# Kernel optimization log

Measured on AMD Instinct MI355X. Metric: run time of the kernel, lower is better.

Reference implementation:

```python
import jax, jax.numpy as jnp
import numpy as np

NODE_NUM = 256  # nodes per env block; N = NODE_NUM * n_thr
N, MAX_DEG, N_FEAT, N_HID, N_CLASS = 8192, 16, 128, 256, 64


def _xavier_uniform(key, fan_in, fan_out, gain=1.414):
    limit = gain * np.sqrt(6.0 / (fan_in + fan_out))
    return jax.random.uniform(key, (fan_in, fan_out), jnp.float32, -limit, limit)


def setup_inputs() -> dict:
    key = jax.random.key(0)
    k1, k2, k3, k4 = jax.random.split(key, 4)
    x = jax.random.normal(k1, (N, N_FEAT), jnp.float32)
    edge_index = jax.random.randint(k2, (N, MAX_DEG), 0, NODE_NUM)  # local neighbor ids, -1 = pad
    W1 = _xavier_uniform(k3, N_FEAT, N_HID)
    W2 = _xavier_uniform(k4, N_HID, N_CLASS)
    return {"x": x, "edge_index": edge_index, "W1": W1, "W2": W2}


def build_adj(edge_index, node_num):
    # Vectorized version of the nested-Python-loop to_adj scatter.
    n, d = edge_index.shape
    rows = jnp.broadcast_to(jnp.arange(n)[:, None], (n, d))  # [N, D]
    cols = edge_index + node_num * (rows // node_num)        # global neighbor index
    valid = (edge_index != -1).astype(jnp.float32)
    # .max with 0 for invalid entries is a no-op regardless of the (wrapped) index,
    # exactly reproducing "set adj[i, j_ind] = 1 only when j != -1".
    adj = jnp.zeros((n, n), jnp.float32).at[rows.ravel(), cols.ravel()].max(valid.ravel())
    return adj


def reference(x, edge_index, W1, W2):
    adj = build_adj(edge_index, NODE_NUM)            # [N, N]
    h = jax.nn.relu(adj @ (x @ W1))                  # gc1 + relu (dropout is identity at eval)
    out = adj @ (h @ W2)                             # gc2
    return jax.nn.log_softmax(out, axis=1)
```

## Files before the change

kernel.cpp:

```cpp
#include <hip/hip_runtime.h>
#include <math.h>

#define NNODES   8192
#define NODE_NUM 256
#define MAX_DEG  16
#define N_FEAT   128
#define N_HID    256
#define N_CLASS  64

#define AG_STRIDE 136
#define HB_STRIDE 264

typedef __attribute__((ext_vector_type(8))) short bf16x8;
typedef __attribute__((ext_vector_type(4))) short s16x4;
typedef __attribute__((ext_vector_type(4))) float f32x4;

static __device__ __forceinline__ short f2b(float f) {
    unsigned u = __float_as_uint(f);
    unsigned r = (u + 0x7fffu + ((u >> 16) & 1u)) >> 16;
    return (short)r;
}
static __device__ __forceinline__ float b2f(short s) {
    return __uint_as_float(((unsigned)(unsigned short)s) << 16);
}

__global__ __launch_bounds__(256) void k_prep(const int* __restrict__ edge,
                                              const float* __restrict__ W1,
                                              const float* __restrict__ W2,
                                              unsigned int* __restrict__ maskw,
                                              short* __restrict__ W1T,
                                              short* __restrict__ W2T) {
    const int g = blockIdx.x * 256 + threadIdx.x;
    if (g < 8192) {
        const int* e = edge + (size_t)g * MAX_DEG;
        int ids[MAX_DEG];
#pragma unroll
        for (int k = 0; k < MAX_DEG; ++k) ids[k] = e[k];
        unsigned m = 0;
#pragma unroll
        for (int k = 0; k < MAX_DEG; ++k) {
            bool skip = (ids[k] == -1);
#pragma unroll
            for (int q = 0; q < k; ++q) skip = skip || (ids[q] == ids[k]);
            if (!skip) m |= 1u << k;
        }
        maskw[g] = m;
    } else if (g < 40960) {
        const int o = g - 8192;
        const int j = o & 7, l = (o >> 3) & 63, k4 = (o >> 9) & 3, nt = (o >> 11) & 15;
        W1T[o] = f2b(W1[(k4 * 32 + (l >> 4) * 8 + j) * N_HID + nt * 16 + (l & 15)]);
    } else if (g < 57344) {
        const int o = g - 40960;
        const int j = o & 7, l = (o >> 3) & 63, k8 = (o >> 9) & 7, nt = (o >> 12) & 3;
        W2T[o] = f2b(W2[(k8 * 32 + (l >> 4) * 8 + j) * N_CLASS + nt * 16 + (l & 15)]);
    }
}

__global__ __launch_bounds__(512) void k_main(const float* __restrict__ x,
                                              const int* __restrict__ edge,
                                              const unsigned int* __restrict__ maskw,
                                              const short* __restrict__ W1T,
                                              const short* __restrict__ W2T,
                                              short* __restrict__ t2b) {
    __shared__ short agg[32 * AG_STRIDE];
    __shared__ short hb[32 * HB_STRIDE];

    const int bid  = blockIdx.x;
    const int work = (bid & 7) * 32 + (bid >> 3);
    const int row0 = work * 32;
    const int t    = threadIdx.x;
    const int w    = t >> 6, l = t & 63;
    const int l16  = l & 15, l4 = l >> 4;

    bf16x8 w1f[4][4];
    {
        const int ntb = (w & 3) * 4;
#pragma unroll
        for (int n = 0; n < 4; ++n)
#pragma unroll
            for (int k4 = 0; k4 < 4; ++k4)
                w1f[n][k4] = *(const bf16x8*)(W1T + ((size_t)((ntb + n) * 4 + k4) * 64 + l) * 8);
    }
    bf16x8 w2f[8];
    {
        const int nt = w & 3;
#pragma unroll
        for (int k8 = 0; k8 < 8; ++k8)
            w2f[k8] = *(const bf16x8*)(W2T + ((size_t)(nt * 8 + k8) * 64 + l) * 8);
    }

    {
        const int r = t >> 4, c = t & 15;
        const int node = row0 + r;
        const int base = node & ~(NODE_NUM - 1);
        const int* e = edge + (size_t)node * MAX_DEG;
        const unsigned m = maskw[node];
        float a[8] = {0, 0, 0, 0, 0, 0, 0, 0};
#pragma unroll
        for (int k = 0; k < MAX_DEG; ++k) {
            const int id = e[k] & (NODE_NUM - 1);
            const float sel = ((m >> k) & 1u) ? 1.0f : 0.0f;
            const float* rowp = x + (size_t)(base + id) * N_FEAT + c * 8;
            float4 v0 = *(const float4*)(rowp);
            float4 v1 = *(const float4*)(rowp + 4);
            a[0] = fmaf(sel, v0.x, a[0]); a[1] = fmaf(sel, v0.y, a[1]);
            a[2] = fmaf(sel, v0.z, a[2]); a[3] = fmaf(sel, v0.w, a[3]);
            a[4] = fmaf(sel, v1.x, a[4]); a[5] = fmaf(sel, v1.y, a[5]);
            a[6] = fmaf(sel, v1.z, a[6]); a[7] = fmaf(sel, v1.w, a[7]);
        }
        bf16x8 p;
#pragma unroll
        for (int j = 0; j < 8; ++j) p[j] = f2b(a[j]);
        *(bf16x8*)(&agg[r * AG_STRIDE + c * 8]) = p;
    }
    __syncthreads();

    const int mt = w >> 2, ntc = w & 3;
    {
        bf16x8 af[4];
#pragma unroll
        for (int k4 = 0; k4 < 4; ++k4)
            af[k4] = *(const bf16x8*)(&agg[(mt * 16 + l16) * AG_STRIDE + k4 * 32 + l4 * 8]);
#pragma unroll
        for (int n = 0; n < 4; ++n) {
            f32x4 acc = {0.f, 0.f, 0.f, 0.f};
#pragma unroll
            for (int k4 = 0; k4 < 4; ++k4)
                acc = __builtin_amdgcn_mfma_f32_16x16x32_bf16(af[k4], w1f[n][k4], acc, 0, 0, 0);
#pragma unroll
            for (int r = 0; r < 4; ++r)
                hb[(mt * 16 + l4 * 4 + r) * HB_STRIDE + (ntc * 4 + n) * 16 + l16] =
                    f2b(fmaxf(acc[r], 0.f));
        }
    }
    __syncthreads();

    {
        f32x4 acc = {0.f, 0.f, 0.f, 0.f};
#pragma unroll
        for (int k8 = 0; k8 < 8; ++k8) {
            bf16x8 a = *(const bf16x8*)(&hb[(mt * 16 + l16) * HB_STRIDE + k8 * 32 + l4 * 8]);
            acc = __builtin_amdgcn_mfma_f32_16x16x32_bf16(a, w2f[k8], acc, 0, 0, 0);
        }
#pragma unroll
        for (int r = 0; r < 4; ++r)
            t2b[(size_t)(row0 + mt * 16 + l4 * 4 + r) * N_CLASS + ntc * 16 + l16] = f2b(acc[r]);
    }
}

__global__ __launch_bounds__(256) void k_final(const short* __restrict__ t2b,
                                               const int* __restrict__ edge,
                                               const unsigned int* __restrict__ maskw,
                                               float* __restrict__ out) {
    const int bid  = blockIdx.x;
    const int work = (bid & 7) * 32 + (bid >> 3);
    const int row0 = work * 32;
    const int t    = threadIdx.x;
    const int r = t >> 3, mm = t & 7;
    const int node = row0 + r;
    const int base = node & ~(NODE_NUM - 1);
    const int* e = edge + (size_t)node * MAX_DEG;
    const unsigned m = maskw[node];

    float acc[8] = {0, 0, 0, 0, 0, 0, 0, 0};
#pragma unroll
    for (int k = 0; k < MAX_DEG; ++k) {
        const int id = e[k] & (NODE_NUM - 1);
        const float sel = ((m >> k) & 1u) ? 1.0f : 0.0f;
        bf16x8 v = *(const bf16x8*)(t2b + (size_t)(base + id) * N_CLASS + mm * 8);
#pragma unroll
        for (int j = 0; j < 8; ++j) acc[j] = fmaf(sel, b2f(v[j]), acc[j]);
    }
    float mx = acc[0];
#pragma unroll
    for (int j = 1; j < 8; ++j) mx = fmaxf(mx, acc[j]);
#pragma unroll
    for (int o = 1; o < 8; o <<= 1) mx = fmaxf(mx, __shfl_xor(mx, o, 64));
    float s = 0.f;
#pragma unroll
    for (int j = 0; j < 8; ++j) s += expf(acc[j] - mx);
#pragma unroll
    for (int o = 1; o < 8; o <<= 1) s += __shfl_xor(s, o, 64);
    const float lse = mx + logf(s);

    float* op = out + (size_t)node * N_CLASS + mm * 8;
    float4 o0 = {acc[0] - lse, acc[1] - lse, acc[2] - lse, acc[3] - lse};
    float4 o1 = {acc[4] - lse, acc[5] - lse, acc[6] - lse, acc[7] - lse};
    *(float4*)(op)     = o0;
    *(float4*)(op + 4) = o1;
}

extern "C" void kernel_launch(void* const* d_in, const int* in_sizes, int n_in,
                              void* d_out, int out_size, void* d_ws, size_t ws_size,
                              hipStream_t stream) {
    const float* x    = (const float*)d_in[0];
    const int*   edge = (const int*)d_in[1];
    const float* W1   = (const float*)d_in[2];
    const float* W2   = (const float*)d_in[3];
    float* out = (float*)d_out;

    char* ws = (char*)d_ws;
    unsigned int* maskw = (unsigned int*)ws;
    short*        W1T   = (short*)(ws + (32 << 10));
    short*        W2T   = (short*)(ws + (96 << 10));
    short*        t2b   = (short*)(ws + (128 << 10));

    k_prep <<<256,         256, 0, stream>>>(edge, W1, W2, maskw, W1T, W2T);
    k_main <<<NNODES / 32, 512, 0, stream>>>(x, edge, maskw, W1T, W2T, t2b);
    k_final<<<NNODES / 32, 256, 0, stream>>>(t2b, edge, maskw, out);
}
```

Baseline: 71.34 us.

## Fold prep kernel into main and final kernels, recomputing masks and weight packing inline

Removes the separate prep launch. Each block of k_main now converts W1/W2 from fp32 to bf16 MFMA fragments itself, using strided global loads. k_main and k_final also recompute the per-node neighbour dedup mask from edge ids instead of reading a precomputed mask. This saves a kernel launch and the serial dependency on it, at the cost of redundant weight conversion in every block, uncoalesced scalar weight loads, and duplicated dedup work in two kernels.

```diff
diff --git a/kernel.cpp b/kernel.cpp
--- a/kernel.cpp
+++ b/kernel.cpp
@@ -12,7 +12,6 @@
 #define HB_STRIDE 264
 
 typedef __attribute__((ext_vector_type(8))) short bf16x8;
-typedef __attribute__((ext_vector_type(4))) short s16x4;
 typedef __attribute__((ext_vector_type(4))) float f32x4;
 
 static __device__ __forceinline__ short f2b(float f) {
@@ -24,43 +23,22 @@
     return __uint_as_float(((unsigned)(unsigned short)s) << 16);
 }
 
-__global__ __launch_bounds__(256) void k_prep(const int* __restrict__ edge,
+static __device__ __forceinline__ unsigned dedup_mask(const int* ids) {
+    unsigned m = 0;
+#pragma unroll
+    for (int k = 0; k < MAX_DEG; ++k) {
+        bool skip = (ids[k] == -1);
+#pragma unroll
+        for (int q = 0; q < k; ++q) skip = skip || (ids[q] == ids[k]);
+        if (!skip) m |= 1u << k;
+    }
+    return m;
+}
+
+__global__ __launch_bounds__(512) void k_main(const float* __restrict__ x,
+                                              const int* __restrict__ edge,
                                               const float* __restrict__ W1,
                                               const float* __restrict__ W2,
-                                              unsigned int* __restrict__ maskw,
-                                              short* __restrict__ W1T,
-                                              short* __restrict__ W2T) {
-    const int g = blockIdx.x * 256 + threadIdx.x;
-    if (g < 8192) {
-        const int* e = edge + (size_t)g * MAX_DEG;
-        int ids[MAX_DEG];
-#pragma unroll
-        for (int k = 0; k < MAX_DEG; ++k) ids[k] = e[k];
-        unsigned m = 0;
-#pragma unroll
-        for (int k = 0; k < MAX_DEG; ++k) {
-            bool skip = (ids[k] == -1);
-#pragma unroll
-            for (int q = 0; q < k; ++q) skip = skip || (ids[q] == ids[k]);
-            if (!skip) m |= 1u << k;
-        }
-        maskw[g] = m;
-    } else if (g < 40960) {
-        const int o = g - 8192;
-        const int j = o & 7, l = (o >> 3) & 63, k4 = (o >> 9) & 3, nt = (o >> 11) & 15;
-        W1T[o] = f2b(W1[(k4 * 32 + (l >> 4) * 8 + j) * N_HID + nt * 16 + (l & 15)]);
-    } else if (g < 57344) {
-        const int o = g - 40960;
-        const int j = o & 7, l = (o >> 3) & 63, k8 = (o >> 9) & 7, nt = (o >> 12) & 3;
-        W2T[o] = f2b(W2[(k8 * 32 + (l >> 4) * 8 + j) * N_CLASS + nt * 16 + (l & 15)]);
-    }
-}
-
-__global__ __launch_bounds__(512) void k_main(const float* __restrict__ x,
-                                              const int* __restrict__ edge,
-                                              const unsigned int* __restrict__ maskw,
-                                              const short* __restrict__ W1T,
-                                              const short* __restrict__ W2T,
                                               short* __restrict__ t2b) {
     __shared__ short agg[32 * AG_STRIDE];
     __shared__ short hb[32 * HB_STRIDE];
@@ -78,15 +56,26 @@
 #pragma unroll
         for (int n = 0; n < 4; ++n)
 #pragma unroll
-            for (int k4 = 0; k4 < 4; ++k4)
-                w1f[n][k4] = *(const bf16x8*)(W1T + ((size_t)((ntb + n) * 4 + k4) * 64 + l) * 8);
+            for (int k4 = 0; k4 < 4; ++k4) {
+                const int col = (ntb + n) * 16 + l16;
+                const int kb  = k4 * 32 + l4 * 8;
+                bf16x8 v;
+#pragma unroll
+                for (int j = 0; j < 8; ++j) v[j] = f2b(W1[(kb + j) * N_HID + col]);
+                w1f[n][k4] = v;
+            }
     }
     bf16x8 w2f[8];
     {
-        const int nt = w & 3;
-#pragma unroll
-        for (int k8 = 0; k8 < 8; ++k8)
-            w2f[k8] = *(const bf16x8*)(W2T + ((size_t)(nt * 8 + k8) * 64 + l) * 8);
+        const int col = (w & 3) * 16 + l16;
+#pragma unroll
+        for (int k8 = 0; k8 < 8; ++k8) {
+            const int kb = k8 * 32 + l4 * 8;
+            bf16x8 v;
+#pragma unroll
+            for (int j = 0; j < 8; ++j) v[j] = f2b(W2[(kb + j) * N_CLASS + col]);
+            w2f[k8] = v;
+        }
     }
 
     {
@@ -94,11 +83,14 @@
         const int node = row0 + r;
         const int base = node & ~(NODE_NUM - 1);
         const int* e = edge + (size_t)node * MAX_DEG;
-        const unsigned m = maskw[node];
+        int ids[MAX_DEG];
+#pragma unroll
+        for (int k = 0; k < MAX_DEG; ++k) ids[k] = e[k];
+        const unsigned m = dedup_mask(ids);
         float a[8] = {0, 0, 0, 0, 0, 0, 0, 0};
 #pragma unroll
         for (int k = 0; k < MAX_DEG; ++k) {
-            const int id = e[k] & (NODE_NUM - 1);
+            const int id = ids[k] & (NODE_NUM - 1);
             const float sel = ((m >> k) & 1u) ? 1.0f : 0.0f;
             const float* rowp = x + (size_t)(base + id) * N_FEAT + c * 8;
             float4 v0 = *(const float4*)(rowp);
@@ -150,7 +142,6 @@
 
 __global__ __launch_bounds__(256) void k_final(const short* __restrict__ t2b,
                                                const int* __restrict__ edge,
-                                               const unsigned int* __restrict__ maskw,
                                                float* __restrict__ out) {
     const int bid  = blockIdx.x;
     const int work = (bid & 7) * 32 + (bid >> 3);
@@ -160,12 +151,15 @@
     const int node = row0 + r;
     const int base = node & ~(NODE_NUM - 1);
     const int* e = edge + (size_t)node * MAX_DEG;
-    const unsigned m = maskw[node];
+    int ids[MAX_DEG];
+#pragma unroll
+    for (int k = 0; k < MAX_DEG; ++k) ids[k] = e[k];
+    const unsigned m = dedup_mask(ids);
 
     float acc[8] = {0, 0, 0, 0, 0, 0, 0, 0};
 #pragma unroll
     for (int k = 0; k < MAX_DEG; ++k) {
-        const int id = e[k] & (NODE_NUM - 1);
+        const int id = ids[k] & (NODE_NUM - 1);
         const float sel = ((m >> k) & 1u) ? 1.0f : 0.0f;
         bf16x8 v = *(const bf16x8*)(t2b + (size_t)(base + id) * N_CLASS + mm * 8);
 #pragma unroll
@@ -199,13 +193,8 @@
     const float* W2   = (const float*)d_in[3];
     float* out = (float*)d_out;
 
-    char* ws = (char*)d_ws;
-    unsigned int* maskw = (unsigned int*)ws;
-    short*        W1T   = (short*)(ws + (32 << 10));
-    short*        W2T   = (short*)(ws + (96 << 10));
-    short*        t2b   = (short*)(ws + (128 << 10));
-
-    k_prep <<<256,         256, 0, stream>>>(edge, W1, W2, maskw, W1T, W2T);
-    k_main <<<NNODES / 32, 512, 0, stream>>>(x, edge, maskw, W1T, W2T, t2b);
-    k_final<<<NNODES / 32, 256, 0, stream>>>(t2b, edge, maskw, out);
-}
+    short* t2b = (short*)d_ws;
+
+    k_main <<<NNODES / 32, 512, 0, stream>>>(x, edge, W1, W2, t2b);
+    k_final<<<NNODES / 32, 256, 0, stream>>>(t2b, edge, out);
+}
```

New measurement: 76.14 us. +6.7%, slower.
